# Optimization experiments

Hardware: AMD Instinct MI355X
Metric: run time of the kernel (lower is better)

## Reference

```python
import jax, jax.numpy as jnp
import numpy as np

W_WIN = 21  # window size (init arg w)
N_HEADS = 8
HEAD_DIM = 64

def setup_inputs() -> dict:
    key = jax.random.key(0)
    ks = jax.random.split(key, 6)
    b, c, l, d = 8, 2, 2048, 512
    x = jax.random.normal(ks[0], (b, c, l, d), dtype=jnp.float32)
    Wqkv = jax.random.normal(ks[1], (d, 3 * d), dtype=jnp.float32) * (1.0 / np.sqrt(d))
    bqkv = jax.random.normal(ks[2], (3 * d,), dtype=jnp.float32) * 0.02
    bias_rw = jax.random.uniform(ks[3], (N_HEADS, HEAD_DIM), dtype=jnp.float32,
                                 minval=-1.0 / np.sqrt(HEAD_DIM), maxval=1.0 / np.sqrt(HEAD_DIM))
    Wout = jax.random.normal(ks[4], (d, d), dtype=jnp.float32) * (1.0 / np.sqrt(d))
    bout = jax.random.normal(ks[5], (d,), dtype=jnp.float32) * 0.02
    return {"x": x, "Wqkv": Wqkv, "bqkv": bqkv, "bias_rw": bias_rw, "Wout": Wout, "bout": bout}

def reference(x, Wqkv, bqkv, bias_rw, Wout, bout):
    b, c, l, d = x.shape
    H, hd = bias_rw.shape
    B = b * c
    w_half = W_WIN // 2

    xf = x.reshape(B, l, d)
    qkv = xf @ Wqkv + bqkv                      # [B, l, 3d]
    q, k, v = jnp.split(qkv, 3, axis=-1)
    q = q.reshape(B, l, H, hd) * (hd ** -0.5)
    k = k.reshape(B, l, H, hd)
    v = v.reshape(B, l, H, hd)

    qk = q + bias_rw                            # bias_r_w added to queries (q_r branch is dead code)

    # banded scores: offset o corresponds to key position p + (o - w_half)
    kp = jnp.pad(k, ((0, 0), (w_half, w_half), (0, 0), (0, 0)))
    vp = jnp.pad(v, ((0, 0), (w_half, w_half), (0, 0), (0, 0)))
    scores = jnp.stack(
        [jnp.einsum('blnh,blnh->bln', qk, jax.lax.dynamic_slice_in_dim(kp, o, l, axis=1))
         for o in range(W_WIN)], axis=-1)       # [B, l, H, w]

    pos = jnp.arange(l)[:, None] + (jnp.arange(W_WIN)[None, :] - w_half)  # [l, w]
    valid = (pos >= 0) & (pos < l)
    neg = -jnp.finfo(scores.dtype).max
    scores = jnp.where(valid[None, :, None, :], scores, neg)

    A = jax.nn.softmax(scores, axis=-1)         # [B, l, H, w]; dropout(0.2) is identity at eval

    z = jnp.zeros_like(v)
    for o in range(W_WIN):
        z = z + A[:, :, :, o, None] * jax.lax.dynamic_slice_in_dim(vp, o, l, axis=1)

    z = z.reshape(b, c, l, H * hd)
    return z @ Wout + bout
```

## Files before the change

### kernel.cpp

```cpp
#include <hip/hip_runtime.h>
#include <stdint.h>

typedef __bf16 bf16x8 __attribute__((ext_vector_type(8)));
typedef float f32x4 __attribute__((ext_vector_type(4)));
typedef unsigned short u16x8 __attribute__((ext_vector_type(8)));

__device__ __forceinline__ unsigned short f2bf(float f) {
  uint32_t u = __builtin_bit_cast(uint32_t, f);
  u += 0x7FFFu + ((u >> 16) & 1u);
  return (unsigned short)(u >> 16);
}
__device__ __forceinline__ float bf2f(unsigned short h) {
  uint32_t u = ((uint32_t)h) << 16;
  return __builtin_bit_cast(float, u);
}

__device__ __forceinline__ void gload_lds16(const void* g, void* l) {
  __builtin_amdgcn_global_load_lds(
      (const __attribute__((address_space(1))) uint32_t*)g,
      (__attribute__((address_space(3))) uint32_t*)l,
      16, 0, 0);
}


__global__ __launch_bounds__(256) void k_cvt_x(const float* __restrict__ x,
                                               unsigned short* __restrict__ xb, int n4) {
  int stride = gridDim.x * blockDim.x;
  for (int i = blockIdx.x * blockDim.x + threadIdx.x; i < n4; i += stride) {
    float4 v = reinterpret_cast<const float4*>(x)[i];
    ushort4 o;
    o.x = f2bf(v.x); o.y = f2bf(v.y); o.z = f2bf(v.z); o.w = f2bf(v.w);
    reinterpret_cast<ushort4*>(xb)[i] = o;
  }
}

__global__ __launch_bounds__(256) void k_cvt_wT(const float* __restrict__ w,
                                                unsigned short* __restrict__ wt, int K, int N) {
  int total = K * N;
  int stride = gridDim.x * blockDim.x;
  for (int i = blockIdx.x * blockDim.x + threadIdx.x; i < total; i += stride) {
    int n = i / K;
    int k = i - n * K;
    wt[i] = f2bf(w[(size_t)k * N + n]);
  }
}

template <int EPI>
__global__ __launch_bounds__(256, 4) void k_gemm128(
    const unsigned short* __restrict__ A,
    const unsigned short* __restrict__ Bt,
    const float* __restrict__ bias,
    const float* __restrict__ brw,
    unsigned short* __restrict__ oq,
    unsigned short* __restrict__ okk,
    unsigned short* __restrict__ ov,
    float* __restrict__ of,
    int Ntiles) {
  __shared__ __align__(128) char lds[32768];

  int cpx = gridDim.x >> 3;
  int bid = (blockIdx.x & 7) * cpx + (blockIdx.x >> 3);
  int bm = bid / Ntiles;
  int bn = bid - bm * Ntiles;
  int row0 = bm << 7;
  int col0 = bn << 7;
  int t = threadIdx.x;
  int lane = t & 63;
  int w = t >> 6;
  int wm = w >> 1;
  int wn = w & 1;
  int lr = lane & 15;
  int lk = lane >> 4;

  const unsigned short* Ab = A + (size_t)row0 * 512;
  const unsigned short* Bb = Bt + (size_t)col0 * 512;

  f32x4 acc[4][4];
#pragma unroll
  for (int i = 0; i < 4; ++i)
#pragma unroll
    for (int j = 0; j < 4; ++j) acc[i][j] = f32x4{0.f, 0.f, 0.f, 0.f};

  auto stage = [&](int kt) {
    int k0 = kt << 5;
    char* base = lds + ((kt & 1) << 14);
#pragma unroll
    for (int i = 0; i < 2; ++i) {
      int o = (i << 8) + t;
      int row = o >> 2;
      int slot = o & 3;
      int gk = k0 + ((slot ^ ((row >> 1) & 3)) << 3);
      gload_lds16(Ab + (size_t)row * 512 + gk, base + (o << 4));
      gload_lds16(Bb + (size_t)row * 512 + gk, base + 8192 + (o << 4));
    }
  };

  auto tile = [&](int kt) {
    const char* Abuf = lds + ((kt & 1) << 14);
    const char* Bbuf = Abuf + 8192;
    bf16x8 af[4], bfs[4];
#pragma unroll
    for (int nf = 0; nf < 4; ++nf) {
      int r = (wn << 6) + (nf << 4) + lr;
      bfs[nf] = *reinterpret_cast<const bf16x8*>(Bbuf + (r << 6) + ((lk ^ ((r >> 1) & 3)) << 4));
    }
#pragma unroll
    for (int mf = 0; mf < 4; ++mf) {
      int r = (wm << 6) + (mf << 4) + lr;
      af[mf] = *reinterpret_cast<const bf16x8*>(Abuf + (r << 6) + ((lk ^ ((r >> 1) & 3)) << 4));
    }
    __builtin_amdgcn_s_setprio(1);
#pragma unroll
    for (int mf = 0; mf < 4; ++mf)
#pragma unroll
      for (int nf = 0; nf < 4; ++nf)
        acc[mf][nf] = __builtin_amdgcn_mfma_f32_16x16x32_bf16(af[mf], bfs[nf], acc[mf][nf], 0, 0, 0);
    __builtin_amdgcn_s_setprio(0);
  };

  stage(0);
  asm volatile("s_waitcnt vmcnt(0)" ::: "memory");
  __builtin_amdgcn_s_barrier();

#pragma unroll 1
  for (int kt = 0; kt < 15; ++kt) {
    stage(kt + 1);
    tile(kt);
    asm volatile("s_waitcnt vmcnt(0)" ::: "memory");
    __builtin_amdgcn_s_barrier();
  }
  tile(15);
  __builtin_amdgcn_s_barrier();

  if (EPI == 0) {
    char* ep = lds + (w << 13);
    int gc0 = col0 + (wn << 6);
    int part = gc0 >> 9;
    int hh = (gc0 & 511) >> 6;
    unsigned short* dst = (part == 0) ? oq : (part == 1) ? okk : ov;
    float bvv[4], rbv[4];
#pragma unroll
    for (int nf = 0; nf < 4; ++nf) {
      int cc = (nf << 4) + lr;
      bvv[nf] = bias[gc0 + cc];
      rbv[nf] = (part == 0) ? brw[(gc0 & 511) + cc] : 0.f;
    }
#pragma unroll
    for (int mf = 0; mf < 4; ++mf) {
#pragma unroll
      for (int nf = 0; nf < 4; ++nf) {
        int cc = (nf << 4) + lr;
#pragma unroll
        for (int j = 0; j < 4; ++j) {
          int r = (mf << 4) + (lk << 2) + j;
          float v = acc[mf][nf][j] + bvv[nf];
          if (part == 0) v = v * 0.125f + rbv[nf];
          int byte = (r << 7) + ((((cc >> 3) ^ (r & 7))) << 4) + ((cc & 7) << 1);
          *reinterpret_cast<unsigned short*>(ep + byte) = f2bf(v);
        }
      }
    }
    asm volatile("s_waitcnt lgkmcnt(0)" ::: "memory");
    __builtin_amdgcn_sched_barrier(0);
    int b0 = row0 >> 11;
    size_t base = (size_t)(b0 * 8 + hh) * 2048;
#pragma unroll
    for (int i = 0; i < 8; ++i) {
      int rr = (i << 3) + (lane >> 3);
      int ch = lane & 7;
      int byte = (rr << 7) + ((ch ^ (rr & 7)) << 4);
      u16x8 val = *reinterpret_cast<const u16x8*>(ep + byte);
      int gl = (row0 + (wm << 6) + rr) & 2047;
      *reinterpret_cast<u16x8*>(dst + ((base + gl) << 6) + (ch << 3)) = val;
    }
  } else {
#pragma unroll
    for (int mf = 0; mf < 4; ++mf) {
#pragma unroll
      for (int j = 0; j < 4; ++j) {
        int gr = row0 + (wm << 6) + (mf << 4) + (lk << 2) + j;
#pragma unroll
        for (int nf = 0; nf < 4; ++nf) {
          int gc = col0 + (wn << 6) + (nf << 4) + lr;
          of[(size_t)gr * 512 + gc] = acc[mf][nf][j] + bias[gc];
        }
      }
    }
  }
}

__global__ __launch_bounds__(256) void k_attn_mfma(
    const unsigned short* __restrict__ qb,
    const unsigned short* __restrict__ kb,
    const unsigned short* __restrict__ vb,
    unsigned short* __restrict__ zb) {
  __shared__ __align__(128) unsigned short smem[13312];

  int t = threadIdx.x;
  int bh = blockIdx.x >> 5;
  int l0 = (blockIdx.x & 31) << 6;
  size_t slab = (size_t)bh << 17;

#pragma unroll
  for (int i = 0; i < 3; ++i) {
    int kloc = (i << 5) + (t >> 3);
    int c8 = (t & 7) << 3;
    int kg = l0 - 10 + kloc;
    kg = kg < 0 ? 0 : (kg > 2047 ? 2047 : kg);
    u16x8 v = *reinterpret_cast<const u16x8*>(vb + slab + ((size_t)kg << 6) + c8);
#pragma unroll
    for (int e = 0; e < 8; ++e) smem[(c8 + e) * 104 + kloc] = v[e];
  }

  int lane = t & 63;
  int w = t >> 6;
  int lr = lane & 15;
  int lk = lane >> 4;

  const unsigned short* qp = qb + slab + ((size_t)(l0 + (w << 4) + lr) << 6) + (lk << 3);
  bf16x8 qf0 = *reinterpret_cast<const bf16x8*>(qp);
  bf16x8 qf1 = *reinterpret_cast<const bf16x8*>(qp + 32);

  f32x4 sacc[6];
#pragma unroll
  for (int kt = 0; kt < 6; ++kt) {
    int kl = (kt << 4) + lr;
    int kg = l0 - 10 + kl;
    int kgc = kg < 0 ? 0 : (kg > 2047 ? 2047 : kg);
    const unsigned short* kp = kb + slab + ((size_t)kgc << 6) + (lk << 3);
    bf16x8 kf0 = *reinterpret_cast<const bf16x8*>(kp);
    bf16x8 kf1 = *reinterpret_cast<const bf16x8*>(kp + 32);
    f32x4 z4 = {0.f, 0.f, 0.f, 0.f};
    z4 = __builtin_amdgcn_mfma_f32_16x16x32_bf16(qf0, kf0, z4, 0, 0, 0);
    sacc[kt] = __builtin_amdgcn_mfma_f32_16x16x32_bf16(qf1, kf1, z4, 0, 0, 0);
  }

  int qlb = (w << 4) + (lk << 2);
  float p[6][4];
  float minv[4];
#pragma unroll
  for (int j = 0; j < 4; ++j) {
    int ql = qlb + j;
    float mx = -1e30f;
#pragma unroll
    for (int kt = 0; kt < 6; ++kt) {
      int kl = (kt << 4) + lr;
      int kg = l0 - 10 + kl;
      bool valid = (kl >= ql) && (kl <= ql + 20) && (kg >= 0) && (kg < 2048);
      float sv = valid ? sacc[kt][j] : -1e30f;
      p[kt][j] = sv;
      mx = fmaxf(mx, sv);
    }
    mx = fmaxf(mx, __shfl_xor(mx, 1));
    mx = fmaxf(mx, __shfl_xor(mx, 2));
    mx = fmaxf(mx, __shfl_xor(mx, 4));
    mx = fmaxf(mx, __shfl_xor(mx, 8));
    float sum = 0.f;
#pragma unroll
    for (int kt = 0; kt < 6; ++kt) {
      float e = (p[kt][j] > -1e29f) ? __expf(p[kt][j] - mx) : 0.f;
      p[kt][j] = e;
      sum += e;
    }
    sum += __shfl_xor(sum, 1);
    sum += __shfl_xor(sum, 2);
    sum += __shfl_xor(sum, 4);
    sum += __shfl_xor(sum, 8);
    minv[j] = 1.f / sum;
  }

  unsigned short* P = smem + 6656;
#pragma unroll
  for (int j = 0; j < 4; ++j)
#pragma unroll
    for (int kt = 0; kt < 6; ++kt)
      P[(qlb + j) * 104 + (kt << 4) + lr] = f2bf(p[kt][j]);

  __syncthreads();

  f32x4 zacc[4];
#pragma unroll
  for (int dt = 0; dt < 4; ++dt) zacc[dt] = f32x4{0.f, 0.f, 0.f, 0.f};
  bf16x8 pf[3];
#pragma unroll
  for (int s3 = 0; s3 < 3; ++s3)
    pf[s3] = *reinterpret_cast<const bf16x8*>(P + ((w << 4) + lr) * 104 + (s3 << 5) + (lk << 3));
#pragma unroll
  for (int dt = 0; dt < 4; ++dt) {
#pragma unroll
    for (int s3 = 0; s3 < 3; ++s3) {
      bf16x8 vf = *reinterpret_cast<const bf16x8*>(smem + ((dt << 4) + lr) * 104 + (s3 << 5) + (lk << 3));
      zacc[dt] = __builtin_amdgcn_mfma_f32_16x16x32_bf16(pf[s3], vf, zacc[dt], 0, 0, 0);
    }
  }

  __syncthreads();

  unsigned short* ZL = smem;
#pragma unroll
  for (int dt = 0; dt < 4; ++dt)
#pragma unroll
    for (int j = 0; j < 4; ++j)
      ZL[(qlb + j) * 80 + (dt << 4) + lr] = f2bf(zacc[dt][j] * minv[j]);
  asm volatile("s_waitcnt lgkmcnt(0)" ::: "memory");
  __builtin_amdgcn_sched_barrier(0);

  int b = bh >> 3, h = bh & 7;
#pragma unroll
  for (int i = 0; i < 2; ++i) {
    int rr = (w << 4) + (i << 3) + (lane >> 3);
    int ch = (lane & 7) << 3;
    u16x8 val = *reinterpret_cast<const u16x8*>(ZL + rr * 80 + ch);
    size_t orow = (size_t)(b * 2048 + l0 + rr);
    *reinterpret_cast<u16x8*>(zb + (orow << 9) + (h << 6) + ch) = val;
  }
}


extern "C" void kernel_launch(void* const* d_in, const int* in_sizes, int n_in,
                              void* d_out, int out_size, void* d_ws, size_t ws_size,
                              hipStream_t stream) {
  (void)in_sizes; (void)n_in; (void)out_size; (void)ws_size;
  const float* x    = (const float*)d_in[0];
  const float* Wqkv = (const float*)d_in[1];
  const float* bqkv = (const float*)d_in[2];
  const float* brw  = (const float*)d_in[3];
  const float* Wout = (const float*)d_in[4];
  const float* bout = (const float*)d_in[5];
  float* out = (float*)d_out;

  char* ws = (char*)d_ws;
  unsigned short* xb  = (unsigned short*)(ws);
  unsigned short* wqT = (unsigned short*)(ws + 33554432);
  unsigned short* woT = (unsigned short*)(ws + 35127296);
  unsigned short* qs  = (unsigned short*)(ws + 35651584);
  unsigned short* kbf = (unsigned short*)(ws + 69206016);
  unsigned short* vbf = (unsigned short*)(ws + 102760448);
  unsigned short* zb  = xb;

  k_cvt_x<<<2048, 256, 0, stream>>>(x, xb, 16777216 / 4);
  k_cvt_wT<<<768, 256, 0, stream>>>(Wqkv, wqT, 512, 1536);
  k_cvt_wT<<<256, 256, 0, stream>>>(Wout, woT, 512, 512);
  k_gemm128<0><<<3072, 256, 0, stream>>>(xb, wqT, bqkv, brw, qs, kbf, vbf, nullptr, 12);
  k_attn_mfma<<<4096, 256, 0, stream>>>(qs, kbf, vbf, zb);
  k_gemm128<1><<<1024, 256, 0, stream>>>(zb, woT, bout, nullptr, nullptr, nullptr, nullptr, out, 4);
}
```

Baseline: 156.9 us.

## Load GEMM B fragments directly from global into registers, bypassing LDS

The B-operand tiles of the 128x128 GEMM are no longer staged through LDS. Each lane now loads its bf16x8 fragments straight from global memory into registers, double-buffered one k-step ahead, and the LDS footprint per stage is halved. This removes the LDS writes and reads for B and the associated bank traffic. In exchange the two wm warps sharing a column range load the same B data redundantly from global or L2, the per-lane loads are strided across rows, and register pressure rises.

Result: slower. 210.9 us (+34.5%).

```diff
diff --git a/kernel.cpp b/kernel.cpp
--- a/kernel.cpp
+++ b/kernel.cpp
@@ -73,7 +73,7 @@
   int lk = lane >> 4;
 
   const unsigned short* Ab = A + (size_t)row0 * 512;
-  const unsigned short* Bb = Bt + (size_t)col0 * 512;
+  const unsigned short* Bp = Bt + (size_t)(col0 + (wn << 6) + lr) * 512 + (lk << 3);
 
   f32x4 acc[4][4];
 #pragma unroll
@@ -81,9 +81,9 @@
 #pragma unroll
     for (int j = 0; j < 4; ++j) acc[i][j] = f32x4{0.f, 0.f, 0.f, 0.f};
 
-  auto stage = [&](int kt) {
+  auto stageA = [&](int kt) {
     int k0 = kt << 5;
-    char* base = lds + ((kt & 1) << 14);
+    char* base = lds + ((kt & 1) << 13);
 #pragma unroll
     for (int i = 0; i < 2; ++i) {
       int o = (i << 8) + t;
@@ -91,45 +91,62 @@
       int slot = o & 3;
       int gk = k0 + ((slot ^ ((row >> 1) & 3)) << 3);
       gload_lds16(Ab + (size_t)row * 512 + gk, base + (o << 4));
-      gload_lds16(Bb + (size_t)row * 512 + gk, base + 8192 + (o << 4));
     }
   };
 
-  auto tile = [&](int kt) {
-    const char* Abuf = lds + ((kt & 1) << 14);
-    const char* Bbuf = Abuf + 8192;
-    bf16x8 af[4], bfs[4];
-#pragma unroll
-    for (int nf = 0; nf < 4; ++nf) {
-      int r = (wn << 6) + (nf << 4) + lr;
-      bfs[nf] = *reinterpret_cast<const bf16x8*>(Bbuf + (r << 6) + ((lk ^ ((r >> 1) & 3)) << 4));
-    }
+  auto loadB = [&](int kt, bf16x8* dst) {
+    const unsigned short* p = Bp + (kt << 5);
+#pragma unroll
+    for (int nf = 0; nf < 4; ++nf)
+      dst[nf] = *reinterpret_cast<const bf16x8*>(p + ((size_t)nf << 13));
+  };
+
+  bf16x8 bcur[4], bnext[4];
+
+  stageA(0);
+  loadB(0, bcur);
+  asm volatile("s_waitcnt vmcnt(0)" ::: "memory");
+  __builtin_amdgcn_s_barrier();
+
+#pragma unroll 1
+  for (int kt = 0; kt < 15; ++kt) {
+    stageA(kt + 1);
+    loadB(kt + 1, bnext);
+    {
+      const char* Abuf = lds + ((kt & 1) << 13);
+      bf16x8 af[4];
+#pragma unroll
+      for (int mf = 0; mf < 4; ++mf) {
+        int r = (wm << 6) + (mf << 4) + lr;
+        af[mf] = *reinterpret_cast<const bf16x8*>(Abuf + (r << 6) + ((lk ^ ((r >> 1) & 3)) << 4));
+      }
+      __builtin_amdgcn_s_setprio(1);
+#pragma unroll
+      for (int mf = 0; mf < 4; ++mf)
+#pragma unroll
+        for (int nf = 0; nf < 4; ++nf)
+          acc[mf][nf] = __builtin_amdgcn_mfma_f32_16x16x32_bf16(af[mf], bcur[nf], acc[mf][nf], 0, 0, 0);
+      __builtin_amdgcn_s_setprio(0);
+    }
+    asm volatile("s_waitcnt vmcnt(0)" ::: "memory");
+    __builtin_amdgcn_s_barrier();
+#pragma unroll
+    for (int nf = 0; nf < 4; ++nf) bcur[nf] = bnext[nf];
+  }
+  {
+    const char* Abuf = lds + ((15 & 1) << 13);
+    bf16x8 af[4];
 #pragma unroll
     for (int mf = 0; mf < 4; ++mf) {
       int r = (wm << 6) + (mf << 4) + lr;
       af[mf] = *reinterpret_cast<const bf16x8*>(Abuf + (r << 6) + ((lk ^ ((r >> 1) & 3)) << 4));
     }
-    __builtin_amdgcn_s_setprio(1);
 #pragma unroll
     for (int mf = 0; mf < 4; ++mf)
 #pragma unroll
       for (int nf = 0; nf < 4; ++nf)
-        acc[mf][nf] = __builtin_amdgcn_mfma_f32_16x16x32_bf16(af[mf], bfs[nf], acc[mf][nf], 0, 0, 0);
-    __builtin_amdgcn_s_setprio(0);
-  };
-
-  stage(0);
-  asm volatile("s_waitcnt vmcnt(0)" ::: "memory");
-  __builtin_amdgcn_s_barrier();
-
-#pragma unroll 1
-  for (int kt = 0; kt < 15; ++kt) {
-    stage(kt + 1);
-    tile(kt);
-    asm volatile("s_waitcnt vmcnt(0)" ::: "memory");
-    __builtin_amdgcn_s_barrier();
-  }
-  tile(15);
+        acc[mf][nf] = __builtin_amdgcn_mfma_f32_16x16x32_bf16(af[mf], bcur[nf], acc[mf][nf], 0, 0, 0);
+  }
   __builtin_amdgcn_s_barrier();
 
   if (EPI == 0) {
```
